# Kernel optimization log

Measured on AMD Instinct MI355X. Metric: run time of the kernel, lower is better.

The kernel has to match this reference:

```python
import jax, jax.numpy as jnp
import numpy as np

IN_DIM = 128
OUT_DIM = 128
B, N = 8, 2048
NEG_SLOPE = 0.2


def setup_inputs() -> dict:
    key = jax.random.key(0)
    k_h, k_adj, k_W, k_a = jax.random.split(key, 4)
    h = jax.random.normal(k_h, (B, N, IN_DIM), dtype=jnp.float32)
    adj = jax.random.randint(k_adj, (B, N, N), 0, 2, dtype=jnp.int32)
    # nn.Linear(in, out, bias=False): weight [out, in]
    W = jax.random.normal(k_W, (OUT_DIM, IN_DIM), dtype=jnp.float32) * (1.0 / np.sqrt(IN_DIM))
    # nn.Linear(2*out, 1, bias=False): weight [1, 2*out] -> store as vector [2*out]
    a = jax.random.normal(k_a, (2 * OUT_DIM,), dtype=jnp.float32) * (1.0 / np.sqrt(2 * OUT_DIM))
    return {"h": h, "adj": adj, "W": W, "a": a}


def reference(h, adj, W, a):
    # Wh: [B, N, Fo]
    Wh = jnp.einsum("bnf,of->bno", h, W)
    Fo = Wh.shape[-1]
    a_src, a_dst = a[:Fo], a[Fo:]
    # attn(cat([Wh_i, Wh_j])) == (Wh_i . a_src) + (Wh_j . a_dst) -- avoids [B,N,N,2F]
    s = Wh @ a_src  # [B, N]
    t = Wh @ a_dst  # [B, N]
    e = jax.nn.leaky_relu(s[:, :, None] + t[:, None, :], negative_slope=NEG_SLOPE)  # [B,N,N]
    e = jnp.where(adj == 0, -jnp.inf, e)
    alpha = jax.nn.softmax(e, axis=-1)
    alpha = jnp.nan_to_num(alpha, nan=0.0)  # rows with no neighbors -> 0
    return jnp.einsum("bnm,bmo->bno", alpha, Wh)
```

## Files before the change

### kernel.cpp

```cpp
#include <hip/hip_runtime.h>
#include <hip/hip_bf16.h>
#include <hip/hip_fp16.h>
#include <math.h>

#define B_ 8
#define N_ 2048
#define F_ 128

typedef __attribute__((ext_vector_type(8))) _Float16 half8;
typedef __attribute__((ext_vector_type(4))) float f32x4;

__global__ __launch_bounds__(256) void k_gemm(
    const float* __restrict__ h, const float* __restrict__ W,
    const float* __restrict__ a,
    _Float16* __restrict__ WhH, float* __restrict__ sv, float* __restrict__ tv)
{
    __shared__ float h_s[64][129];
    __shared__ float Wt[128][68];
    __shared__ float wsm[128], wtm[128];
    __shared__ float sred[64][4], tred[64][4];

    const int t = threadIdx.x;
    const int rowblk = blockIdx.x >> 1;
    const int ohalf  = blockIdx.x & 1;
    const int r0 = rowblk * 64;

    {
        const int f = (t & 31) * 4;
        #pragma unroll
        for (int it = 0; it < 8; ++it) {
            const int r = (t >> 5) + it * 8;
            float4 v = *(const float4*)&h[(size_t)(r0 + r) * F_ + f];
            h_s[r][f] = v.x; h_s[r][f + 1] = v.y;
            h_s[r][f + 2] = v.z; h_s[r][f + 3] = v.w;
        }
    }
    {
        const int f = (t & 31) * 4;
        #pragma unroll
        for (int it = 0; it < 8; ++it) {
            const int o = (t >> 5) + it * 8;
            float4 v = *(const float4*)&W[(size_t)(ohalf * 64 + o) * F_ + f];
            Wt[f][o] = v.x; Wt[f + 1][o] = v.y;
            Wt[f + 2][o] = v.z; Wt[f + 3][o] = v.w;
        }
    }
    {
        const int f = t & 127;
        const int which = t >> 7;
        const float* av = a + which * 128;
        float acc = 0.f;
        for (int o = 0; o < 128; ++o)
            acc += W[(size_t)o * F_ + f] * av[o];
        if (which == 0) wsm[f] = acc; else wtm[f] = acc;
    }
    __syncthreads();

    const int o4 = t & 15;
    const int r4 = t >> 4;
    float acc[4][4];
    #pragma unroll
    for (int i = 0; i < 4; ++i)
        #pragma unroll
        for (int j = 0; j < 4; ++j) acc[i][j] = 0.f;

    #pragma unroll 4
    for (int k = 0; k < 128; ++k) {
        float4 w = *(const float4*)&Wt[k][o4 * 4];
        float h0 = h_s[r4 * 4 + 0][k];
        float h1 = h_s[r4 * 4 + 1][k];
        float h2 = h_s[r4 * 4 + 2][k];
        float h3 = h_s[r4 * 4 + 3][k];
        acc[0][0] += h0 * w.x; acc[0][1] += h0 * w.y; acc[0][2] += h0 * w.z; acc[0][3] += h0 * w.w;
        acc[1][0] += h1 * w.x; acc[1][1] += h1 * w.y; acc[1][2] += h1 * w.z; acc[1][3] += h1 * w.w;
        acc[2][0] += h2 * w.x; acc[2][1] += h2 * w.y; acc[2][2] += h2 * w.z; acc[2][3] += h2 * w.w;
        acc[3][0] += h3 * w.x; acc[3][1] += h3 * w.y; acc[3][2] += h3 * w.z; acc[3][3] += h3 * w.w;
    }

    {
        const int Rbase = r0 + r4 * 4;
        const int b    = Rbase >> 11;
        const int jj   = Rbase & 2047;
        const int jblk = jj >> 5;
        const int k8   = (jj >> 3) & 3;
        const int kk   = jj & 7;
        #pragma unroll
        for (int jo = 0; jo < 4; ++jo) {
            const int o = ohalf * 64 + o4 * 4 + jo;
            size_t off = ((size_t)(b * 64 + jblk) * 128 + o) * 32 + k8 * 8 + kk;
            union { _Float16 x[4]; uint2 u; } pk;
            pk.x[0] = (_Float16)acc[0][jo];
            pk.x[1] = (_Float16)acc[1][jo];
            pk.x[2] = (_Float16)acc[2][jo];
            pk.x[3] = (_Float16)acc[3][jo];
            *(uint2*)(WhH + off) = pk.u;
        }
    }

    {
        const int r = t & 63, part = t >> 6;
        float as_ = 0.f, at_ = 0.f;
        const int kb = part * 32;
        for (int k = kb; k < kb + 32; ++k) {
            float hv = h_s[r][k];
            as_ += hv * wsm[k];
            at_ += hv * wtm[k];
        }
        sred[r][part] = as_; tred[r][part] = at_;
    }
    __syncthreads();
    if (ohalf == 0 && t < 64) {
        sv[r0 + t] = sred[t][0] + sred[t][1] + sred[t][2] + sred[t][3];
        tv[r0 + t] = tred[t][0] + tred[t][1] + tred[t][2] + tred[t][3];
    }
}

__global__ __launch_bounds__(256, 3) void k_attn(
    const _Float16* __restrict__ WhH, const float* __restrict__ sv,
    const float* __restrict__ tv, const int* __restrict__ adj,
    float* __restrict__ Po, float* __restrict__ Pl)
{
    __shared__ _Float16 whS[2][4096];
    __shared__ float tS[512];
    __shared__ float tmr[4];

    const int t   = threadIdx.x;
    const int b   = blockIdx.x & 7;
    const int rem = blockIdx.x >> 3;
    const int i0  = (rem & 31) * 64;
    const int jh  = rem >> 5;
    const int jbase = jh * 512;

    const float* tb = tv + ((size_t)b << 11);

    float tm = -INFINITY;
    #pragma unroll
    for (int k = 0; k < 8; ++k) tm = fmaxf(tm, tb[t + k * 256]);
    #pragma unroll
    for (int k = 32; k; k >>= 1) tm = fmaxf(tm, __shfl_xor(tm, k, 64));
    if ((t & 63) == 0) tmr[t >> 6] = tm;

    tS[t]       = tb[jbase + t];
    tS[t + 256] = tb[jbase + t + 256];

    const int wv   = t >> 6;
    const int lane = t & 63;
    const int m_   = lane & 15;
    const int q_   = lane >> 4;

    const int   girow = (b << 11) + i0 + wv * 16 + m_;
    const float s_i   = sv[girow];
    const int*  arow  = adj + ((size_t)girow << 11) + jbase + q_ * 8;

    const _Float16* whc = WhH + (((size_t)b * 64 + jh * 16) << 12);

    {
        uint4 w0 = *(const uint4*)(whc + (size_t)t * 8);
        uint4 w1 = *(const uint4*)(whc + (size_t)(t + 256) * 8);
        *(uint4*)&whS[0][t * 8]         = w0;
        *(uint4*)&whS[0][(t + 256) * 8] = w1;
    }
    int4 aC0 = *(const int4*)(arow);
    int4 aC1 = *(const int4*)(arow + 4);
    __syncthreads();
    const float M_i = fmaxf(s_i + fmaxf(fmaxf(tmr[0], tmr[1]), fmaxf(tmr[2], tmr[3])), 0.f);

    f32x4 acc[8];
    #pragma unroll
    for (int n = 0; n < 8; ++n) acc[n] = (f32x4){0.f, 0.f, 0.f, 0.f};
    float lsum = 0.f;

    for (int jj = 0; jj < 16; ++jj) {
        const int cur  = jj & 1;
        const int nxt  = (jj + 1) & 15;
        const int nbuf = (jj + 1) & 1;

        const _Float16* whn = whc + ((size_t)nxt << 12);
        uint4 w0 = *(const uint4*)(whn + (size_t)t * 8);
        uint4 w1 = *(const uint4*)(whn + (size_t)(t + 256) * 8);
        int4 aN0 = *(const int4*)(arow + nxt * 32);
        int4 aN1 = *(const int4*)(arow + nxt * 32 + 4);

        float4 tL = *(const float4*)&tS[jj * 32 + q_ * 8];
        float4 tH = *(const float4*)&tS[jj * 32 + q_ * 8 + 4];
        float tvk[8] = {tL.x, tL.y, tL.z, tL.w, tH.x, tH.y, tH.z, tH.w};
        int   avk[8] = {aC0.x, aC0.y, aC0.z, aC0.w, aC1.x, aC1.y, aC1.z, aC1.w};
        half8 af;
        #pragma unroll
        for (int k = 0; k < 8; ++k) {
            float e = s_i + tvk[k]; e = fmaxf(e, 0.2f * e);
            float p = avk[k] ? __expf(e - M_i) : 0.f;
            lsum += p;
            af[k] = (_Float16)p;
        }

        #pragma unroll
        for (int n = 0; n < 8; ++n) {
            half8 bf = *(const half8*)&whS[cur][n * 512 + m_ * 32 + q_ * 8];
            acc[n] = __builtin_amdgcn_mfma_f32_16x16x32_f16(af, bf, acc[n], 0, 0, 0);
        }

        __syncthreads();
        *(uint4*)&whS[nbuf][t * 8]         = w0;
        *(uint4*)&whS[nbuf][(t + 256) * 8] = w1;
        aC0 = aN0; aC1 = aN1;
        __syncthreads();
    }

    lsum += __shfl_xor(lsum, 16, 64);
    lsum += __shfl_xor(lsum, 32, 64);
    if (q_ == 0) Pl[(size_t)jh * (B_ * N_) + girow] = lsum;

    float* po = Po + (size_t)jh * ((size_t)B_ * N_ * F_)
              + (((size_t)((b << 11) + i0 + wv * 16)) << 7);
    #pragma unroll
    for (int n = 0; n < 8; ++n)
        #pragma unroll
        for (int r = 0; r < 4; ++r)
            po[(size_t)(q_ * 4 + r) * F_ + n * 16 + m_] = acc[n][r];
}

__global__ __launch_bounds__(256) void k_comb(
    const float* __restrict__ Po, const float* __restrict__ Pl,
    float* __restrict__ out)
{
    const int idx = blockIdx.x * 256 + threadIdx.x;
    const int gi  = idx >> 5;
    const int o4  = (idx & 31) * 4;
    const size_t stride = (size_t)B_ * N_ * F_;

    float4 v = *(const float4*)&Po[(size_t)gi * F_ + o4];
    float  l = Pl[gi];
    #pragma unroll
    for (int jh = 1; jh < 4; ++jh) {
        float4 u = *(const float4*)&Po[jh * stride + (size_t)gi * F_ + o4];
        v.x += u.x; v.y += u.y; v.z += u.z; v.w += u.w;
        l += Pl[jh * (B_ * N_) + gi];
    }
    const float sc = l > 0.f ? 1.f / l : 0.f;
    float4 r = {v.x * sc, v.y * sc, v.z * sc, v.w * sc};
    *(float4*)&out[(size_t)gi * F_ + o4] = r;
}

extern "C" void kernel_launch(void* const* d_in, const int* in_sizes, int n_in,
                              void* d_out, int out_size, void* d_ws, size_t ws_size,
                              hipStream_t stream) {
    const float* h   = (const float*)d_in[0];
    const int*   adj = (const int*)d_in[1];
    const float* W   = (const float*)d_in[2];
    const float* a   = (const float*)d_in[3];
    float* out = (float*)d_out;

    char* ws = (char*)d_ws;
    _Float16* WhH = (_Float16*)ws;
    float* sv = (float*)(ws + (size_t)4 * 1024 * 1024);
    float* tv = sv + (size_t)B_ * N_;
    float* Po = (float*)(ws + (size_t)8 * 1024 * 1024);
    float* Pl = (float*)(ws + (size_t)40 * 1024 * 1024);

    k_gemm<<<512, 256, 0, stream>>>(h, W, a, WhH, sv, tv);
    k_attn<<<1024, 256, 0, stream>>>(WhH, sv, tv, adj, Po, Pl);
    k_comb<<<2048, 256, 0, stream>>>(Po, Pl, out);
}
```

Before: 235.1 us.

## Stream adjacency and Wh tiles directly into LDS via global_load_lds

The attention kernel now issues asynchronous global-to-LDS loads for both the fp16 Wh tiles and the int32 adjacency tiles, instead of staging them through registers. Adjacency is double-buffered in shared memory with an XOR swizzle applied on the global side, then read back per lane. This drops one barrier per iteration and frees registers, and the occupancy hint goes from 3 to 4 blocks per CU. The cost is extra LDS use. Correctness also depends on the barrier waiting for the outstanding direct-to-LDS loads.

```diff
diff --git a/kernel.cpp b/kernel.cpp
--- a/kernel.cpp
+++ b/kernel.cpp
@@ -9,6 +9,13 @@
 
 typedef __attribute__((ext_vector_type(8))) _Float16 half8;
 typedef __attribute__((ext_vector_type(4))) float f32x4;
+
+__device__ __forceinline__ void gl2lds16(const void* g, void* l)
+{
+    __builtin_amdgcn_global_load_lds(
+        (const __attribute__((address_space(1))) unsigned int*)g,
+        (__attribute__((address_space(3))) unsigned int*)l, 16, 0, 0);
+}
 
 __global__ __launch_bounds__(256) void k_gemm(
     const float* __restrict__ h, const float* __restrict__ W,
@@ -115,14 +122,15 @@
     }
 }
 
-__global__ __launch_bounds__(256, 3) void k_attn(
+__global__ __launch_bounds__(256, 4) void k_attn(
     const _Float16* __restrict__ WhH, const float* __restrict__ sv,
     const float* __restrict__ tv, const int* __restrict__ adj,
     float* __restrict__ Po, float* __restrict__ Pl)
 {
     __shared__ _Float16 whS[2][4096];
-    __shared__ float tS[512];
-    __shared__ float tmr[4];
+    __shared__ int      adjS[2][2048];
+    __shared__ float    tS[512];
+    __shared__ float    tmr[4];
 
     const int t   = threadIdx.x;
     const int b   = blockIdx.x & 7;
@@ -150,20 +158,28 @@
 
     const int   girow = (b << 11) + i0 + wv * 16 + m_;
     const float s_i   = sv[girow];
-    const int*  arow  = adj + ((size_t)girow << 11) + jbase + q_ * 8;
-
-    const _Float16* whc = WhH + (((size_t)b * 64 + jh * 16) << 12);
-
-    {
-        uint4 w0 = *(const uint4*)(whc + (size_t)t * 8);
-        uint4 w1 = *(const uint4*)(whc + (size_t)(t + 256) * 8);
-        *(uint4*)&whS[0][t * 8]         = w0;
-        *(uint4*)&whS[0][(t + 256) * 8] = w1;
-    }
-    int4 aC0 = *(const int4*)(arow);
-    int4 aC1 = *(const int4*)(arow + 4);
+
+    const int*      adjb = adj + ((size_t)((b << 11) + i0) << 11) + jbase;
+    const _Float16* whc  = WhH + (((size_t)b * 64 + jh * 16) << 12);
+
+    const int s0 = t, s1 = t + 256;
+    const int r0_ = s0 >> 3, g0 = (s0 & 7) ^ (r0_ & 7);
+    const int r1_ = s1 >> 3, g1 = (s1 & 7) ^ (r1_ & 7);
+    const int* a0p = adjb + (size_t)r0_ * N_ + g0 * 4;
+    const int* a1p = adjb + (size_t)r1_ * N_ + g1 * 4;
+
+    gl2lds16(whc + s0 * 8, &whS[0][s0 * 8]);
+    gl2lds16(whc + s1 * 8, &whS[0][s1 * 8]);
+    gl2lds16(a0p,          &adjS[0][s0 * 4]);
+    gl2lds16(a1p,          &adjS[0][s1 * 4]);
     __syncthreads();
-    const float M_i = fmaxf(s_i + fmaxf(fmaxf(tmr[0], tmr[1]), fmaxf(tmr[2], tmr[3])), 0.f);
+
+    const float tmax = fmaxf(fmaxf(tmr[0], tmr[1]), fmaxf(tmr[2], tmr[3]));
+    const float M_i  = fmaxf(s_i + tmax, 0.f);
+
+    const int r_  = wv * 16 + m_;
+    const int sl0 = r_ * 8 + ((2 * q_)     ^ (r_ & 7));
+    const int sl1 = r_ * 8 + ((2 * q_ + 1) ^ (r_ & 7));
 
     f32x4 acc[8];
     #pragma unroll
@@ -171,20 +187,22 @@
     float lsum = 0.f;
 
     for (int jj = 0; jj < 16; ++jj) {
-        const int cur  = jj & 1;
-        const int nxt  = (jj + 1) & 15;
-        const int nbuf = (jj + 1) & 1;
+        const int cur = jj & 1;
+        const int nxt = (jj + 1) & 15;
 
         const _Float16* whn = whc + ((size_t)nxt << 12);
-        uint4 w0 = *(const uint4*)(whn + (size_t)t * 8);
-        uint4 w1 = *(const uint4*)(whn + (size_t)(t + 256) * 8);
-        int4 aN0 = *(const int4*)(arow + nxt * 32);
-        int4 aN1 = *(const int4*)(arow + nxt * 32 + 4);
-
+        const int joff = nxt * 32;
+        gl2lds16(whn + s0 * 8,  &whS[cur ^ 1][s0 * 8]);
+        gl2lds16(whn + s1 * 8,  &whS[cur ^ 1][s1 * 8]);
+        gl2lds16(a0p + joff,    &adjS[cur ^ 1][s0 * 4]);
+        gl2lds16(a1p + joff,    &adjS[cur ^ 1][s1 * 4]);
+
+        int4 aA = *(const int4*)&adjS[cur][sl0 * 4];
+        int4 aB = *(const int4*)&adjS[cur][sl1 * 4];
         float4 tL = *(const float4*)&tS[jj * 32 + q_ * 8];
         float4 tH = *(const float4*)&tS[jj * 32 + q_ * 8 + 4];
         float tvk[8] = {tL.x, tL.y, tL.z, tL.w, tH.x, tH.y, tH.z, tH.w};
-        int   avk[8] = {aC0.x, aC0.y, aC0.z, aC0.w, aC1.x, aC1.y, aC1.z, aC1.w};
+        int   avk[8] = {aA.x, aA.y, aA.z, aA.w, aB.x, aB.y, aB.z, aB.w};
         half8 af;
         #pragma unroll
         for (int k = 0; k < 8; ++k) {
@@ -200,10 +218,6 @@
             acc[n] = __builtin_amdgcn_mfma_f32_16x16x32_f16(af, bf, acc[n], 0, 0, 0);
         }
 
-        __syncthreads();
-        *(uint4*)&whS[nbuf][t * 8]         = w0;
-        *(uint4*)&whS[nbuf][(t + 256) * 8] = w1;
-        aC0 = aN0; aC1 = aN1;
         __syncthreads();
     }
 
```

Result: no change. 235.2 us (+0.1%).
